# Kernel optimization log

Hardware: AMD Instinct MI355X
Metric: run time of the kernel (lower is better)

## Reference

```python
import jax, jax.numpy as jnp
import numpy as np

B, S, R, E, H = 2, 256, 2048, 1024, 16
D = E // H
ROPE_BASE = 10000.0

_PN = ["sum_q", "sum_k", "sum_v", "sum_out", "reg_q", "reg_k", "reg_v", "reg_out", "sum_k2", "sum_v2"]


def setup_inputs() -> dict:
    key = jax.random.key(0)
    ks = jax.random.split(key, 2 + 2 * len(_PN))
    inp = {
        "sum_x": jax.random.normal(ks[0], (B, S, E), jnp.float32),
        "reg_x": jax.random.normal(ks[1], (B, R, E), jnp.float32),
        "ss_mask": jnp.ones((B, S, S), bool),
        "sr_mask": jnp.ones((B, S, R), bool),
        "rs_mask": jnp.ones((B, R, S), bool),
        "rr_mask": jnp.ones((B, R, R), bool),
    }
    for i, n in enumerate(_PN):
        inp[f"W_{n}"] = jax.random.normal(ks[2 + 2 * i], (E, E), jnp.float32) * 0.02
        inp[f"b_{n}"] = jax.random.normal(ks[3 + 2 * i], (E,), jnp.float32) * 0.02
    return inp


def _lin(x, W, b):
    return x @ W.T + b


def _heads(x):  # (B, L, E) -> (B, H, L, D)
    b, l, _ = x.shape
    return x.reshape(b, l, H, D).transpose(0, 2, 1, 3)


def _merge(x):  # (B, H, L, D) -> (B, L, E)
    b, _, l, _ = x.shape
    return x.transpose(0, 2, 1, 3).reshape(b, l, E)


def _rope_cos_sin(total_len):
    inv_freq = 1.0 / (ROPE_BASE ** (jnp.arange(0, D, 2, dtype=jnp.float32) / D))
    t = jnp.arange(total_len, dtype=jnp.float32)
    freqs = jnp.outer(t, inv_freq)
    emb = jnp.concatenate([freqs, freqs], axis=-1)  # (total_len, D)
    return jnp.cos(emb)[None, None], jnp.sin(emb)[None, None]


def _rotate_half(x):
    x1, x2 = jnp.split(x, 2, axis=-1)
    return jnp.concatenate([-x2, x1], axis=-1)


def _apply_rope(q, k, cos, sin):
    return q * cos + _rotate_half(q) * sin, k * cos + _rotate_half(k) * sin


def _attn(q, k, v, mask):  # mask: (B, Lq, Lk) bool
    scale = D ** -0.5
    scores = jnp.einsum('bhqd,bhkd->bhqk', q, k) * scale
    scores = jnp.where(mask[:, None, :, :], scores, -jnp.inf)
    p = jax.nn.softmax(scores, axis=-1)
    return jnp.einsum('bhqk,bhkd->bhqd', p, v)


def summary_attention(sum_x, reg_x, ss_mask, sr_mask, rs_mask, rr_mask, params):
    sum_len, reg_len = sum_x.shape[1], reg_x.shape[1]
    sum_q = _heads(_lin(sum_x, params["W_sum_q"], params["b_sum_q"]))
    sum_k = _heads(_lin(sum_x, params["W_sum_k"], params["b_sum_k"]))
    sum_v = _heads(_lin(sum_x, params["W_sum_v"], params["b_sum_v"]))
    reg_q = _heads(_lin(reg_x, params["W_reg_q"], params["b_reg_q"]))
    reg_k = _heads(_lin(reg_x, params["W_reg_k"], params["b_reg_k"]))
    reg_v = _heads(_lin(reg_x, params["W_reg_v"], params["b_reg_v"]))

    cos, sin = _rope_cos_sin(sum_len + reg_len)
    sum_q, sum_k = _apply_rope(sum_q, sum_k, cos[:, :, :sum_len], sin[:, :, :sum_len])
    reg_q, reg_k = _apply_rope(reg_q, reg_k, cos[:, :, sum_len:], sin[:, :, sum_len:])

    # Stage 1: summary queries over [summary, regular] keys
    src_k = jnp.concatenate([sum_k, reg_k], axis=2)
    src_v = jnp.concatenate([sum_v, reg_v], axis=2)
    sx_mask = jnp.concatenate([ss_mask, sr_mask], axis=-1)
    sum_attn_out = _merge(_attn(sum_q, src_k, src_v, sx_mask))  # (B, S, E)

    # Second projection of summarized tokens
    sum_k2 = _heads(_lin(sum_attn_out, params["W_sum_k2"], params["b_sum_k2"]))
    sum_v2 = _heads(_lin(sum_attn_out, params["W_sum_v2"], params["b_sum_v2"]))

    # Stage 2: regular queries over [summary2, regular] keys
    src_k2 = jnp.concatenate([sum_k2, reg_k], axis=2)
    src_v2 = jnp.concatenate([sum_v2, reg_v], axis=2)
    rx_mask = jnp.concatenate([rs_mask, rr_mask], axis=-1)
    reg_attn_out = _merge(_attn(reg_q, src_k2, src_v2, rx_mask))  # (B, R, E)

    sum_output = _lin(sum_attn_out, params["W_sum_out"], params["b_sum_out"])
    reg_output = _lin(reg_attn_out, params["W_reg_out"], params["b_reg_out"])
    return sum_output, reg_output


def reference(sum_x, reg_x, ss_mask, sr_mask, rs_mask, rr_mask,
              W_sum_q, b_sum_q, W_sum_k, b_sum_k, W_sum_v, b_sum_v,
              W_sum_out, b_sum_out, W_reg_q, b_reg_q, W_reg_k, b_reg_k,
              W_reg_v, b_reg_v, W_reg_out, b_reg_out, W_sum_k2, b_sum_k2,
              W_sum_v2, b_sum_v2):
    params = dict(W_sum_q=W_sum_q, b_sum_q=b_sum_q, W_sum_k=W_sum_k, b_sum_k=b_sum_k,
                  W_sum_v=W_sum_v, b_sum_v=b_sum_v, W_sum_out=W_sum_out, b_sum_out=b_sum_out,
                  W_reg_q=W_reg_q, b_reg_q=b_reg_q, W_reg_k=W_reg_k, b_reg_k=b_reg_k,
                  W_reg_v=W_reg_v, b_reg_v=b_reg_v, W_reg_out=W_reg_out, b_reg_out=b_reg_out,
                  W_sum_k2=W_sum_k2, b_sum_k2=b_sum_k2, W_sum_v2=W_sum_v2, b_sum_v2=b_sum_v2)
    return summary_attention(sum_x, reg_x, ss_mask, sr_mask, rs_mask, rr_mask, params)
```

## Files before the change

kernel.cpp:

```cpp
#include <hip/hip_runtime.h>
#include <math.h>

#define SUMSZ 524288
#define REGSZ 4194304
#define CSCALE 0.18033688f

typedef unsigned short us;
typedef __attribute__((ext_vector_type(8))) short short8;
typedef __attribute__((ext_vector_type(4))) float f32x4;

__device__ __forceinline__ us f2bf(float f) {
    unsigned u = __builtin_bit_cast(unsigned, f);
    u += 0x7FFF + ((u >> 16) & 1);
    return (us)(u >> 16);
}
__device__ __forceinline__ float fast_exp2(float x) {
    return __builtin_amdgcn_exp2f(x);
}
__device__ __forceinline__ unsigned pack_trunc(float a, float b, float& qa, float& qb) {
    unsigned ua = __builtin_bit_cast(unsigned, a);
    unsigned ub = __builtin_bit_cast(unsigned, b);
    qa = __builtin_bit_cast(float, ua & 0xffff0000u);
    qb = __builtin_bit_cast(float, ub & 0xffff0000u);
    return (ub & 0xffff0000u) | (ua >> 16);
}

struct GArgs {
    const us* A0; const us* A1;
    const us* W[6]; const float* bias[6]; void* C[6];
    int flag[6];
    int rope[6];
    float scale[6];
    const float* tab;
    int xsplit, Lmask0, Lmask1;
};

template<int BM>
__global__ __launch_bounds__(256) void gemm6_kernel(GArgs a)
{
    constexpr int TI = (BM == 128) ? 4 : 2;
    const int tid = threadIdx.x;
    const int l = tid & 63, w = tid >> 6;
    const int col = l & 15, g = l >> 4;
    const int wm = w >> 1, wn = w & 1;
    const int part = (blockIdx.x >= a.xsplit) ? 1 : 0;
    const int m0 = (part ? (blockIdx.x - a.xsplit) : blockIdx.x) * BM;
    const us* A = part ? a.A1 : a.A0;
    const int Lmask = part ? a.Lmask1 : a.Lmask0;
    const int nG = blockIdx.y * 128;
    const int set = part * 3 + (nG >> 10);
    const int n0 = nG & 1023;
    const us* W = a.W[set];
    const float* bias = a.bias[set];
    void* C = a.C[set];
    const int flag = a.flag[set];
    const int rope = a.rope[set];
    const float scl = a.scale[set];
    const float* tab = a.tab;

    __shared__ us As[(BM / 16) * 512];
    __shared__ us Bs[4096];

    f32x4 acc[TI][4];
    #pragma unroll
    for (int i = 0; i < TI; ++i)
        #pragma unroll
        for (int j = 0; j < 4; ++j) acc[i][j] = (f32x4){0.f, 0.f, 0.f, 0.f};

    const us* ga = A + (size_t)(m0 + w * 16 + col) * 1024 + g * 8;
    const us* gb = W + (size_t)(n0 + w * 16 + col) * 1024 + g * 8;

    short8 pa0, pa1, pb0, pb1;
    auto ld = [&](int kt) {
        pa0 = *(const short8*)(ga + kt);
        if constexpr (BM == 128) pa1 = *(const short8*)(ga + 65536 + kt);
        pb0 = *(const short8*)(gb + kt);
        pb1 = *(const short8*)(gb + 65536 + kt);
    };
    ld(0);

    for (int kt = 0; kt < 1024; kt += 32) {
        __syncthreads();
        *(short8*)&As[w * 512 + l * 8] = pa0;
        if constexpr (BM == 128) *(short8*)&As[(w + 4) * 512 + l * 8] = pa1;
        *(short8*)&Bs[w * 512 + l * 8] = pb0;
        *(short8*)&Bs[(w + 4) * 512 + l * 8] = pb1;
        __syncthreads();
        if (kt + 32 < 1024) ld(kt + 32);

        short8 af[TI], bfr[4];
        #pragma unroll
        for (int i = 0; i < TI; ++i) af[i]  = *(const short8*)&As[(wm * TI + i) * 512 + l * 8];
        #pragma unroll
        for (int j = 0; j < 4; ++j) bfr[j] = *(const short8*)&Bs[(wn * 4 + j) * 512 + l * 8];
        #pragma unroll
        for (int i = 0; i < TI; ++i)
            #pragma unroll
            for (int j = 0; j < 4; ++j)
                acc[i][j] = __builtin_amdgcn_mfma_f32_16x16x32_bf16(af[i], bfr[j], acc[i][j], 0, 0, 0);
    }

    float bv0 = bias[n0 + wn * 64 +  0 + col];
    float bv1 = bias[n0 + wn * 64 + 16 + col];
    float bv2 = bias[n0 + wn * 64 + 32 + col];
    float bv3 = bias[n0 + wn * 64 + 48 + col];
    #pragma unroll
    for (int i = 0; i < TI; ++i) {
        #pragma unroll
        for (int r = 0; r < 4; ++r) {
            int row = m0 + wm * (TI * 16) + i * 16 + g * 4 + r;
            float a0 = acc[i][0][r] + bv0;
            float a1 = acc[i][1][r] + bv1;
            float a2 = acc[i][2][r] + bv2;
            float a3 = acc[i][3][r] + bv3;
            if (rope >= 0) {
                int pos = (row & Lmask) + rope;
                float c0 = tab[(pos * 32 + col) * 2],      s0 = tab[(pos * 32 + col) * 2 + 1];
                float c1 = tab[(pos * 32 + col + 16) * 2], s1 = tab[(pos * 32 + col + 16) * 2 + 1];
                float n0v = a0 * c0 - a2 * s0;
                float n1v = a1 * c1 - a3 * s1;
                float n2v = a2 * c0 + a0 * s0;
                float n3v = a3 * c1 + a1 * s1;
                a0 = n0v; a1 = n1v; a2 = n2v; a3 = n3v;
            }
            a0 *= scl; a1 *= scl; a2 *= scl; a3 *= scl;
            size_t base = (size_t)row * 1024 + n0 + wn * 64 + col;
            if (flag) {
                us* Ch = (us*)C;
                Ch[base]      = f2bf(a0);
                Ch[base + 16] = f2bf(a1);
                Ch[base + 32] = f2bf(a2);
                Ch[base + 48] = f2bf(a3);
            } else {
                float* Cf = (float*)C;
                Cf[base] = a0; Cf[base + 16] = a1; Cf[base + 32] = a2; Cf[base + 48] = a3;
            }
        }
    }
}

__global__ __launch_bounds__(256) void vtrans2_kernel(
    const us* __restrict__ src0, us* __restrict__ dst0, int L0, int xsplit,
    const us* __restrict__ src1, us* __restrict__ dst1, int L1)
{
    const int part = (blockIdx.x >= xsplit) ? 1 : 0;
    const int t = part ? (blockIdx.x - xsplit) : blockIdx.x;
    const us* src = part ? src1 : src0;
    us* dst = part ? dst1 : dst0;
    const int L = part ? L1 : L0;
    const int h = blockIdx.y, b = blockIdx.z;
    __shared__ us T[64][72];
    const int tid = threadIdx.x;
    {
        int key = tid >> 2, seg = (tid & 3) * 16;
        const us* sp = src + ((size_t)b * L + t * 64 + key) * 1024 + h * 64 + seg;
        short8 v0 = *(const short8*)sp;
        short8 v1 = *(const short8*)(sp + 8);
        int kp = (key & 15) * 4 + (key >> 4);
        #pragma unroll
        for (int j = 0; j < 8; ++j) {
            T[seg + j][kp]     = (us)v0[j];
            T[seg + 8 + j][kp] = (us)v1[j];
        }
    }
    __syncthreads();
    {
        int d = tid >> 2, ks = (tid & 3) * 16;
        us* dp = dst + (((size_t)(b * 16 + h) * 64) + d) * L + t * 64 + ks;
        *(short8*)dp       = *(const short8*)&T[d][ks];
        *(short8*)(dp + 8) = *(const short8*)&T[d][ks + 8];
    }
}

template<int NQ, int SPLIT>
__global__ __launch_bounds__(256) void attn5_kernel(
    const us* __restrict__ Q,
    const us* __restrict__ K1, const us* __restrict__ Vt1, int L1,
    const us* __restrict__ K2, const us* __restrict__ Vt2, int L2,
    us* __restrict__ O, float* __restrict__ PO, float* __restrict__ PL, int Lq)
{
    const int tid = threadIdx.x;
    const int l = tid & 63, w = tid >> 6;
    const int col = l & 15, g = l >> 4;
    const int h = blockIdx.y, b = blockIdx.z;
    const int split = blockIdx.x & (SPLIT - 1);
    const int qt = blockIdx.x / SPLIT;

    __shared__ us Ks[8 * 512];
    __shared__ us Vs[8 * 512];
    __shared__ us Ps[4][NQ * 16 * 72];

    const int rowbase = qt * (NQ * 64) + w * (NQ * 16);

    short8 aq[NQ][2];
    #pragma unroll
    for (int qi = 0; qi < NQ; ++qi) {
        const us* qp = Q + ((size_t)b * Lq + rowbase + qi * 16 + col) * 1024 + h * 64 + g * 8;
        aq[qi][0] = *(const short8*)qp;
        aq[qi][1] = *(const short8*)(qp + 32);
    }

    f32x4 o[NQ][4];
    float lsum[NQ][4];
    #pragma unroll
    for (int qi = 0; qi < NQ; ++qi)
        #pragma unroll
        for (int u = 0; u < 4; ++u) { o[qi][u] = (f32x4){0.f,0.f,0.f,0.f}; lsum[qi][u] = 0.f; }

    const int nt1 = L1 >> 6;
    const int ntt = nt1 + (L2 >> 6);
    const int tpb = ntt / SPLIT;
    const int t0 = split * tpb, t1 = t0 + tpb;

    auto tload = [&](int t, short8* pk, short8* pv) {
        const us *Kg, *Vg; int Lv, kb;
        if (t < nt1) {
            Kg = K1 + ((size_t)b * L1 + t * 64) * 1024 + h * 64;
            Vg = Vt1 + (size_t)(b * 16 + h) * 64 * L1;
            Lv = L1; kb = t * 64;
        } else {
            Kg = K2 + ((size_t)b * L2 + (t - nt1) * 64) * 1024 + h * 64;
            Vg = Vt2 + (size_t)(b * 16 + h) * 64 * L2;
            Lv = L2; kb = (t - nt1) * 64;
        }
        const us* gp = Kg + (size_t)(w * 16 + col) * 1024 + g * 8;
        pk[0] = *(const short8*)gp;
        pk[1] = *(const short8*)(gp + 32);
        const us* vp = Vg + (size_t)(w * 16 + col) * Lv + kb + g * 8;
        pv[0] = *(const short8*)vp;
        pv[1] = *(const short8*)(vp + 32);
    };

    short8 pk[2], pv[2];
    tload(t0, pk, pv);

    for (int t = t0; t < t1; ++t) {
        __syncthreads();
        *(short8*)&Ks[(w * 2 + 0) * 512 + l * 8] = pk[0];
        *(short8*)&Ks[(w * 2 + 1) * 512 + l * 8] = pk[1];
        *(short8*)&Vs[(w * 2 + 0) * 512 + l * 8] = pv[0];
        *(short8*)&Vs[(w * 2 + 1) * 512 + l * 8] = pv[1];
        __syncthreads();
        if (t + 1 < t1) tload(t + 1, pk, pv);

        short8 kf[8], vb[8];
        #pragma unroll
        for (int f = 0; f < 8; ++f) kf[f] = *(const short8*)&Ks[f * 512 + l * 8];
        #pragma unroll
        for (int f = 0; f < 8; ++f) vb[f] = *(const short8*)&Vs[f * 512 + l * 8];

        #pragma unroll
        for (int qi = 0; qi < NQ; ++qi) {
            f32x4 s0 = {0.f,0.f,0.f,0.f}, s1 = s0, s2 = s0, s3 = s0;
            s0 = __builtin_amdgcn_mfma_f32_16x16x32_bf16(aq[qi][0], kf[0], s0, 0, 0, 0);
            s0 = __builtin_amdgcn_mfma_f32_16x16x32_bf16(aq[qi][1], kf[1], s0, 0, 0, 0);
            s1 = __builtin_amdgcn_mfma_f32_16x16x32_bf16(aq[qi][0], kf[2], s1, 0, 0, 0);
            s1 = __builtin_amdgcn_mfma_f32_16x16x32_bf16(aq[qi][1], kf[3], s1, 0, 0, 0);
            s2 = __builtin_amdgcn_mfma_f32_16x16x32_bf16(aq[qi][0], kf[4], s2, 0, 0, 0);
            s2 = __builtin_amdgcn_mfma_f32_16x16x32_bf16(aq[qi][1], kf[5], s2, 0, 0, 0);
            s3 = __builtin_amdgcn_mfma_f32_16x16x32_bf16(aq[qi][0], kf[6], s3, 0, 0, 0);
            s3 = __builtin_amdgcn_mfma_f32_16x16x32_bf16(aq[qi][1], kf[7], s3, 0, 0, 0);

            #pragma unroll
            for (int r = 0; r < 4; ++r) {
                float p0 = fast_exp2(s0[r]);
                float p1 = fast_exp2(s1[r]);
                float p2 = fast_exp2(s2[r]);
                float p3 = fast_exp2(s3[r]);
                float q0, q1, q2, q3;
                uint2 pkk;
                pkk.x = pack_trunc(p0, p1, q0, q1);
                pkk.y = pack_trunc(p2, p3, q2, q3);
                lsum[qi][r] += (q0 + q1) + (q2 + q3);
                *(uint2*)&Ps[w][(qi * 16 + g * 4 + r) * 72 + col * 4] = pkk;
            }
        }

        #pragma unroll
        for (int qi = 0; qi < NQ; ++qi) {
            short8 ap0 = *(const short8*)&Ps[w][(qi * 16 + col) * 72 + g * 8];
            short8 ap1 = *(const short8*)&Ps[w][(qi * 16 + col) * 72 + 32 + g * 8];
            o[qi][0] = __builtin_amdgcn_mfma_f32_16x16x32_bf16(ap0, vb[0], o[qi][0], 0, 0, 0);
            o[qi][0] = __builtin_amdgcn_mfma_f32_16x16x32_bf16(ap1, vb[1], o[qi][0], 0, 0, 0);
            o[qi][1] = __builtin_amdgcn_mfma_f32_16x16x32_bf16(ap0, vb[2], o[qi][1], 0, 0, 0);
            o[qi][1] = __builtin_amdgcn_mfma_f32_16x16x32_bf16(ap1, vb[3], o[qi][1], 0, 0, 0);
            o[qi][2] = __builtin_amdgcn_mfma_f32_16x16x32_bf16(ap0, vb[4], o[qi][2], 0, 0, 0);
            o[qi][2] = __builtin_amdgcn_mfma_f32_16x16x32_bf16(ap1, vb[5], o[qi][2], 0, 0, 0);
            o[qi][3] = __builtin_amdgcn_mfma_f32_16x16x32_bf16(ap0, vb[6], o[qi][3], 0, 0, 0);
            o[qi][3] = __builtin_amdgcn_mfma_f32_16x16x32_bf16(ap1, vb[7], o[qi][3], 0, 0, 0);
        }
    }

    #pragma unroll
    for (int qi = 0; qi < NQ; ++qi)
        #pragma unroll
        for (int r = 0; r < 4; ++r) {
            float v = lsum[qi][r];
            v += __shfl_xor(v, 1);
            v += __shfl_xor(v, 2);
            v += __shfl_xor(v, 4);
            v += __shfl_xor(v, 8);
            lsum[qi][r] = v;
        }

    if (SPLIT == 1) {
        #pragma unroll
        for (int qi = 0; qi < NQ; ++qi)
            #pragma unroll
            for (int r = 0; r < 4; ++r) {
                float inv = 1.0f / lsum[qi][r];
                size_t off = ((size_t)b * Lq + rowbase + qi * 16 + g * 4 + r) * 1024 + h * 64 + col;
                O[off]      = f2bf(o[qi][0][r] * inv);
                O[off + 16] = f2bf(o[qi][1][r] * inv);
                O[off + 32] = f2bf(o[qi][2][r] * inv);
                O[off + 48] = f2bf(o[qi][3][r] * inv);
            }
    } else {
        float* po = PO + (size_t)split * ((size_t)2 * Lq * 1024);
        float* pl = PL + split * (2 * Lq * 16);
        #pragma unroll
        for (int qi = 0; qi < NQ; ++qi)
            #pragma unroll
            for (int r = 0; r < 4; ++r) {
                int qr = rowbase + qi * 16 + g * 4 + r;
                size_t off = ((size_t)b * Lq + qr) * 1024 + h * 64 + col;
                po[off]      = o[qi][0][r];
                po[off + 16] = o[qi][1][r];
                po[off + 32] = o[qi][2][r];
                po[off + 48] = o[qi][3][r];
                if (col == 0) pl[(b * Lq + qr) * 16 + h] = lsum[qi][r];
            }
    }
}

__global__ __launch_bounds__(256) void combine_kernel(const float* __restrict__ po,
    const float* __restrict__ pl, us* __restrict__ out)
{
    int idx = blockIdx.x * 256 + threadIdx.x;
    int row = idx >> 10, c = idx & 1023, h = c >> 6;
    float lv = 0.f, ov = 0.f;
    #pragma unroll
    for (int s = 0; s < 4; ++s) {
        lv += pl[s * 8192 + row * 16 + h];
        ov += po[s * 524288 + idx];
    }
    out[idx] = f2bf(ov / lv);
}

__global__ __launch_bounds__(256) void cvt_flat_kernel(
    const float* s0, const float* s1, const float* s2, const float* s3,
    const float* s4, const float* s5, const float* s6, const float* s7,
    const float* s8, const float* s9, const float* s10, const float* s11,
    us* __restrict__ dst, float* __restrict__ tab)
{
    if (blockIdx.x >= 14848) {
        int idx = (blockIdx.x - 14848) * 256 + threadIdx.x;
        int pos = idx >> 5, j = idx & 31;
        float invf = fast_exp2((float)j * -0.41524101f);
        float ang = (float)pos * invf;
        float s, c;
        sincosf(ang, &s, &c);
        tab[idx * 2]     = c;
        tab[idx * 2 + 1] = s;
        return;
    }
    size_t e = (size_t)blockIdx.x * 1024 + threadIdx.x * 4;
    const float* src;
    size_t off;
    if (e < 10485760) {
        const float* ws[10] = {s0,s1,s2,s3,s4,s5,s6,s7,s8,s9};
        src = ws[e >> 20]; off = e & 1048575;
    } else if (e < 11010048) {
        src = s10; off = e - 10485760;
    } else {
        src = s11; off = e - 11010048;
    }
    float4 v = *(const float4*)(src + off);
    us o[4] = {f2bf(v.x), f2bf(v.y), f2bf(v.z), f2bf(v.w)};
    *(uint2*)(dst + e) = *(uint2*)o;
}

extern "C" void kernel_launch(void* const* d_in, const int* in_sizes, int n_in,
                              void* d_out, int out_size, void* d_ws, size_t ws_size,
                              hipStream_t stream)
{
    (void)in_sizes; (void)n_in; (void)out_size; (void)ws_size;

    const float* sum_x_f  = (const float*)d_in[0];
    const float* reg_x_f  = (const float*)d_in[1];
    const float* W_sum_q  = (const float*)d_in[6];  const float* b_sum_q  = (const float*)d_in[7];
    const float* W_sum_k  = (const float*)d_in[8];  const float* b_sum_k  = (const float*)d_in[9];
    const float* W_sum_v  = (const float*)d_in[10]; const float* b_sum_v  = (const float*)d_in[11];
    const float* W_sum_out= (const float*)d_in[12]; const float* b_sum_out= (const float*)d_in[13];
    const float* W_reg_q  = (const float*)d_in[14]; const float* b_reg_q  = (const float*)d_in[15];
    const float* W_reg_k  = (const float*)d_in[16]; const float* b_reg_k  = (const float*)d_in[17];
    const float* W_reg_v  = (const float*)d_in[18]; const float* b_reg_v  = (const float*)d_in[19];
    const float* W_reg_out= (const float*)d_in[20]; const float* b_reg_out= (const float*)d_in[21];
    const float* W_sum_k2 = (const float*)d_in[22]; const float* b_sum_k2 = (const float*)d_in[23];
    const float* W_sum_v2 = (const float*)d_in[24]; const float* b_sum_v2 = (const float*)d_in[25];

    float* out0 = (float*)d_out;
    float* out1 = out0 + SUMSZ;

    us* ws16     = (us*)d_ws;
    us* Wh       = ws16;
    us* xsh      = Wh + 10485760;
    us* xrh      = xsh + SUMSZ;
    us* sum_q    = xrh + REGSZ;
    us* sum_k    = sum_q + SUMSZ;
    us* sum_v    = sum_k + SUMSZ;
    us* sum_attn = sum_v + SUMSZ;
    us* sum_k2   = sum_attn + SUMSZ;
    us* sum_v2   = sum_k2 + SUMSZ;
    us* reg_q    = sum_v2 + SUMSZ;
    us* reg_k    = reg_q + REGSZ;
    us* reg_v    = reg_k + REGSZ;
    us* reg_attn = reg_v + REGSZ;
    us* VtS1     = reg_attn + REGSZ;
    float* tab   = (float*)(VtS1 + SUMSZ);
    float* po    = tab + 147456;
    float* pl    = po + 4 * 524288;
    us* VtR      = xrh;
    us* VtS2     = (us*)po;

    cvt_flat_kernel<<<15136, 256, 0, stream>>>(
        W_sum_q, W_sum_k, W_sum_v, W_sum_out, W_reg_q, W_reg_k, W_reg_v, W_reg_out,
        W_sum_k2, W_sum_v2, sum_x_f, reg_x_f, ws16, tab);

    {
        GArgs a{};
        a.A0 = xsh; a.A1 = xrh; a.xsplit = 4; a.Lmask0 = 255; a.Lmask1 = 2047;
        a.tab = tab;
        a.W[0] = Wh + 0u*1048576; a.bias[0] = b_sum_q; a.C[0] = sum_q; a.flag[0] = 1; a.rope[0] = 0;   a.scale[0] = 1.0f;
        a.W[1] = Wh + 1u*1048576; a.bias[1] = b_sum_k; a.C[1] = sum_k; a.flag[1] = 1; a.rope[1] = 0;   a.scale[1] = CSCALE;
        a.W[2] = Wh + 2u*1048576; a.bias[2] = b_sum_v; a.C[2] = sum_v; a.flag[2] = 1; a.rope[2] = -1;  a.scale[2] = 1.0f;
        a.W[3] = Wh + 4u*1048576; a.bias[3] = b_reg_q; a.C[3] = reg_q; a.flag[3] = 1; a.rope[3] = 256; a.scale[3] = 1.0f;
        a.W[4] = Wh + 5u*1048576; a.bias[4] = b_reg_k; a.C[4] = reg_k; a.flag[4] = 1; a.rope[4] = 256; a.scale[4] = CSCALE;
        a.W[5] = Wh + 6u*1048576; a.bias[5] = b_reg_v; a.C[5] = reg_v; a.flag[5] = 1; a.rope[5] = -1;  a.scale[5] = 1.0f;
        gemm6_kernel<128><<<dim3(36, 24), 256, 0, stream>>>(a);
    }

    vtrans2_kernel<<<dim3(36, 16, 2), 256, 0, stream>>>(
        sum_v, VtS1, 256, 4, reg_v, VtR, 2048);

    attn5_kernel<2, 4><<<dim3(8, 16, 2), 256, 0, stream>>>(
        sum_q, sum_k, VtS1, 256, reg_k, VtR, 2048, nullptr, po, pl, 256);
    combine_kernel<<<2048, 256, 0, stream>>>(po, pl, sum_attn);

    {
        GArgs a{};
        a.A0 = sum_attn; a.A1 = sum_attn; a.xsplit = 8; a.Lmask0 = 255; a.Lmask1 = 255;
        a.tab = tab;
        a.W[0] = Wh + 8u*1048576; a.bias[0] = b_sum_k2; a.C[0] = sum_k2; a.flag[0] = 1; a.rope[0] = -1; a.scale[0] = CSCALE;
        a.W[1] = Wh + 9u*1048576; a.bias[1] = b_sum_v2; a.C[1] = sum_v2; a.flag[1] = 1; a.rope[1] = -1; a.scale[1] = 1.0f;
        a.W[2] = Wh + 3u*1048576; a.bias[2] = b_sum_out;a.C[2] = out0;   a.flag[2] = 0; a.rope[2] = -1; a.scale[2] = 1.0f;
        a.W[3] = a.W[0]; a.bias[3] = a.bias[0]; a.C[3] = a.C[0]; a.flag[3] = 1; a.rope[3] = -1; a.scale[3] = 1.0f;
        a.W[4] = a.W[0]; a.bias[4] = a.bias[0]; a.C[4] = a.C[0]; a.flag[4] = 1; a.rope[4] = -1; a.scale[4] = 1.0f;
        a.W[5] = a.W[0]; a.bias[5] = a.bias[0]; a.C[5] = a.C[0]; a.flag[5] = 1; a.rope[5] = -1; a.scale[5] = 1.0f;
        gemm6_kernel<64><<<dim3(8, 24), 256, 0, stream>>>(a);
    }

    vtrans2_kernel<<<dim3(4, 16, 2), 256, 0, stream>>>(
        sum_v2, VtS2, 256, 4, sum_v2, VtS2, 256);

    attn5_kernel<2, 1><<<dim3(16, 16, 2), 256, 0, stream>>>(
        reg_q, sum_k2, VtS2, 256, reg_k, VtR, 2048, reg_attn, nullptr, nullptr, 2048);

    {
        GArgs a{};
        a.A0 = reg_attn; a.A1 = reg_attn; a.xsplit = 64; a.Lmask0 = 2047; a.Lmask1 = 2047;
        a.tab = tab;
        a.W[0] = Wh + 7u*1048576; a.bias[0] = b_reg_out; a.C[0] = out1; a.flag[0] = 0; a.rope[0] = -1; a.scale[0] = 1.0f;
        for (int s = 1; s < 6; ++s) {
            a.W[s] = a.W[0]; a.bias[s] = a.bias[0]; a.C[s] = a.C[0];
            a.flag[s] = 0; a.rope[s] = -1; a.scale[s] = 1.0f;
        }
        gemm6_kernel<64><<<dim3(64, 8), 256, 0, stream>>>(a);
    }
}
```

Before: 368.9 us.

## Use direct global-to-LDS async loads with double-buffered shared tiles in GEMM and attention

Both the projection GEMM and the attention kernel previously prefetched the next tile into registers and then copied it into shared memory. That needed two barriers per iteration. The new code issues global_load_lds 16-byte loads straight into a second LDS buffer and alternates buffers, leaving one barrier per iteration and no register staging. This doubles the LDS tile footprint and relies on the barrier waiting for the outstanding async loads, which could reduce occupancy or add wait stalls.

```diff
diff --git a/kernel.cpp b/kernel.cpp
--- a/kernel.cpp
+++ b/kernel.cpp
@@ -23,6 +23,12 @@
     qa = __builtin_bit_cast(float, ua & 0xffff0000u);
     qb = __builtin_bit_cast(float, ub & 0xffff0000u);
     return (ub & 0xffff0000u) | (ua >> 16);
+}
+
+typedef const __attribute__((address_space(1))) unsigned int gu32;
+typedef __attribute__((address_space(3))) unsigned int lu32;
+__device__ __forceinline__ void gld16(const us* g, us* l) {
+    __builtin_amdgcn_global_load_lds((gu32*)g, (lu32*)l, 16, 0, 0);
 }
 
 struct GArgs {
@@ -58,8 +64,8 @@
     const float scl = a.scale[set];
     const float* tab = a.tab;
 
-    __shared__ us As[(BM / 16) * 512];
-    __shared__ us Bs[4096];
+    __shared__ us As[2][(BM / 16) * 512];
+    __shared__ us Bs[2][4096];
 
     f32x4 acc[TI][4];
     #pragma unroll
@@ -70,34 +76,30 @@
     const us* ga = A + (size_t)(m0 + w * 16 + col) * 1024 + g * 8;
     const us* gb = W + (size_t)(n0 + w * 16 + col) * 1024 + g * 8;
 
-    short8 pa0, pa1, pb0, pb1;
-    auto ld = [&](int kt) {
-        pa0 = *(const short8*)(ga + kt);
-        if constexpr (BM == 128) pa1 = *(const short8*)(ga + 65536 + kt);
-        pb0 = *(const short8*)(gb + kt);
-        pb1 = *(const short8*)(gb + 65536 + kt);
+    auto stage = [&](int bi, int kt) {
+        gld16(ga + kt, &As[bi][w * 512]);
+        if constexpr (BM == 128) gld16(ga + 65536 + kt, &As[bi][(w + 4) * 512]);
+        gld16(gb + kt, &Bs[bi][w * 512]);
+        gld16(gb + 65536 + kt, &Bs[bi][(w + 4) * 512]);
     };
-    ld(0);
-
+    stage(0, 0);
+
+    int buf = 0;
     for (int kt = 0; kt < 1024; kt += 32) {
         __syncthreads();
-        *(short8*)&As[w * 512 + l * 8] = pa0;
-        if constexpr (BM == 128) *(short8*)&As[(w + 4) * 512 + l * 8] = pa1;
-        *(short8*)&Bs[w * 512 + l * 8] = pb0;
-        *(short8*)&Bs[(w + 4) * 512 + l * 8] = pb1;
-        __syncthreads();
-        if (kt + 32 < 1024) ld(kt + 32);
+        if (kt + 32 < 1024) stage(buf ^ 1, kt + 32);
 
         short8 af[TI], bfr[4];
         #pragma unroll
-        for (int i = 0; i < TI; ++i) af[i]  = *(const short8*)&As[(wm * TI + i) * 512 + l * 8];
-        #pragma unroll
-        for (int j = 0; j < 4; ++j) bfr[j] = *(const short8*)&Bs[(wn * 4 + j) * 512 + l * 8];
+        for (int i = 0; i < TI; ++i) af[i]  = *(const short8*)&As[buf][(wm * TI + i) * 512 + l * 8];
+        #pragma unroll
+        for (int j = 0; j < 4; ++j) bfr[j] = *(const short8*)&Bs[buf][(wn * 4 + j) * 512 + l * 8];
         #pragma unroll
         for (int i = 0; i < TI; ++i)
             #pragma unroll
             for (int j = 0; j < 4; ++j)
                 acc[i][j] = __builtin_amdgcn_mfma_f32_16x16x32_bf16(af[i], bfr[j], acc[i][j], 0, 0, 0);
+        buf ^= 1;
     }
 
     float bv0 = bias[n0 + wn * 64 +  0 + col];
@@ -186,8 +188,8 @@
     const int split = blockIdx.x & (SPLIT - 1);
     const int qt = blockIdx.x / SPLIT;
 
-    __shared__ us Ks[8 * 512];
-    __shared__ us Vs[8 * 512];
+    __shared__ us Ks[2][8 * 512];
+    __shared__ us Vs[2][8 * 512];
     __shared__ us Ps[4][NQ * 16 * 72];
 
     const int rowbase = qt * (NQ * 64) + w * (NQ * 16);
@@ -212,7 +214,7 @@
     const int tpb = ntt / SPLIT;
     const int t0 = split * tpb, t1 = t0 + tpb;
 
-    auto tload = [&](int t, short8* pk, short8* pv) {
+    auto stage = [&](int bi, int t) {
         const us *Kg, *Vg; int Lv, kb;
         if (t < nt1) {
             Kg = K1 + ((size_t)b * L1 + t * 64) * 1024 + h * 64;
@@ -224,30 +226,24 @@
             Lv = L2; kb = (t - nt1) * 64;
         }
         const us* gp = Kg + (size_t)(w * 16 + col) * 1024 + g * 8;
-        pk[0] = *(const short8*)gp;
-        pk[1] = *(const short8*)(gp + 32);
+        gld16(gp,      &Ks[bi][(w * 2 + 0) * 512]);
+        gld16(gp + 32, &Ks[bi][(w * 2 + 1) * 512]);
         const us* vp = Vg + (size_t)(w * 16 + col) * Lv + kb + g * 8;
-        pv[0] = *(const short8*)vp;
-        pv[1] = *(const short8*)(vp + 32);
+        gld16(vp,      &Vs[bi][(w * 2 + 0) * 512]);
+        gld16(vp + 32, &Vs[bi][(w * 2 + 1) * 512]);
     };
-
-    short8 pk[2], pv[2];
-    tload(t0, pk, pv);
-
+    stage(0, t0);
+
+    int buf = 0;
     for (int t = t0; t < t1; ++t) {
         __syncthreads();
-        *(short8*)&Ks[(w * 2 + 0) * 512 + l * 8] = pk[0];
-        *(short8*)&Ks[(w * 2 + 1) * 512 + l * 8] = pk[1];
-        *(short8*)&Vs[(w * 2 + 0) * 512 + l * 8] = pv[0];
-        *(short8*)&Vs[(w * 2 + 1) * 512 + l * 8] = pv[1];
-        __syncthreads();
-        if (t + 1 < t1) tload(t + 1, pk, pv);
+        if (t + 1 < t1) stage(buf ^ 1, t + 1);
 
         short8 kf[8], vb[8];
         #pragma unroll
-        for (int f = 0; f < 8; ++f) kf[f] = *(const short8*)&Ks[f * 512 + l * 8];
-        #pragma unroll
-        for (int f = 0; f < 8; ++f) vb[f] = *(const short8*)&Vs[f * 512 + l * 8];
+        for (int f = 0; f < 8; ++f) kf[f] = *(const short8*)&Ks[buf][f * 512 + l * 8];
+        #pragma unroll
+        for (int f = 0; f < 8; ++f) vb[f] = *(const short8*)&Vs[buf][f * 512 + l * 8];
 
         #pragma unroll
         for (int qi = 0; qi < NQ; ++qi) {
@@ -289,6 +285,7 @@
             o[qi][3] = __builtin_amdgcn_mfma_f32_16x16x32_bf16(ap0, vb[6], o[qi][3], 0, 0, 0);
             o[qi][3] = __builtin_amdgcn_mfma_f32_16x16x32_bf16(ap1, vb[7], o[qi][3], 0, 0, 0);
         }
+        buf ^= 1;
     }
 
     #pragma unroll
```

Measured after the change: 391.4 us. 1.06x slower.
